# Performance work log

Hardware: AMD Instinct MI355X
Metric: run time of the kernel (lower is better)

## Reference

```python
import jax, jax.numpy as jnp
import numpy as np

EPS = 1e-5
NUM_HEADS = 8

def _bn(x, w, b, m, v):
    # inference-mode BatchNorm2d over channel dim of (B,C,H,W)
    inv = w / jnp.sqrt(v + EPS)
    return x * inv[None, :, None, None] + (b - m * inv)[None, :, None, None]

def _conv1x1(x, W, b):
    # 1x1 conv == per-pixel matmul: W is (out_ch, in_ch)
    return jnp.einsum('bchw,ec->behw', x, W) + b[None, :, None, None]

def _forward(x, bn1_w, bn1_b, bn1_m, bn1_v, Wq, bq, Wk, bk, Wv, bv, gamma, temperature,
             conv_w, conv_b, cbn_w, cbn_b, cbn_m, cbn_v, rs_w, rs_b, rbn_w, rbn_b, rbn_m, rbn_v):
    B, C, Wd, Hd = x.shape
    S = Wd * Hd
    E = Wq.shape[0]
    hd = E // NUM_HEADS
    xa = jax.nn.relu(_bn(x, bn1_w, bn1_b, bn1_m, bn1_v))
    def proj(Wm, bm):
        return _conv1x1(xa, Wm, bm).reshape(B, NUM_HEADS, hd, S).transpose(0, 1, 3, 2)  # (B,h,S,d)
    q = proj(Wq, bq)
    k = proj(Wk, bk)
    v = proj(Wv, bv)
    scores = jnp.einsum('bhsd,bhtd->bhst', q, k) / temperature  # (B,h,S,S)
    scores = scores - jnp.max(scores, axis=-1, keepdims=True)   # redundant amax-subtract as in source
    attn = jax.nn.softmax(scores, axis=-1)
    out = jnp.einsum('bhst,bhtd->bhsd', attn, v)
    out = out.transpose(0, 1, 3, 2).reshape(B, E, Wd, Hd)
    conv_path = jax.nn.relu(_bn(_conv1x1(x, conv_w, conv_b), cbn_w, cbn_b, cbn_m, cbn_v))
    fused = gamma[0] * out + conv_path
    return jax.nn.gelu(_bn(_conv1x1(fused, rs_w, rs_b), rbn_w, rbn_b, rbn_m, rbn_v), approximate=False)

def setup_inputs() -> dict:
    key = jax.random.key(0)
    ks = jax.random.split(key, 18)
    C, E = 256, 512
    n = lambda k, s, sc=0.02: jax.random.normal(k, s, jnp.float32) * sc
    return {
        'x': jax.random.normal(ks[0], (1, C, 64, 64), jnp.float32),
        'bn1_w': 1.0 + n(ks[1], (C,), 0.1), 'bn1_b': n(ks[2], (C,), 0.1),
        'bn1_m': n(ks[3], (C,), 0.05), 'bn1_v': 0.5 + jax.random.uniform(ks[4], (C,), jnp.float32),
        'Wq': n(ks[5], (E, C)), 'bq': jnp.zeros((E,), jnp.float32),
        'Wk': n(ks[6], (E, C)), 'bk': jnp.zeros((E,), jnp.float32),
        'Wv': n(ks[7], (E, C)), 'bv': jnp.zeros((E,), jnp.float32),
        'gamma': jnp.full((1,), 0.5, jnp.float32),
        'temperature': jnp.asarray(0.85, jnp.float32),
        'conv_w': n(ks[8], (E, C)), 'conv_b': jnp.zeros((E,), jnp.float32),
        'cbn_w': 1.0 + n(ks[9], (E,), 0.1), 'cbn_b': n(ks[10], (E,), 0.1),
        'cbn_m': n(ks[11], (E,), 0.05), 'cbn_v': 0.5 + jax.random.uniform(ks[12], (E,), jnp.float32),
        'rs_w': n(ks[13], (C, E)), 'rs_b': jnp.zeros((C,), jnp.float32),
        'rbn_w': 1.0 + n(ks[14], (C,), 0.1), 'rbn_b': n(ks[15], (C,), 0.1),
        'rbn_m': n(ks[16], (C,), 0.05), 'rbn_v': 0.5 + jax.random.uniform(ks[17], (C,), jnp.float32),
    }

def reference(x, bn1_w, bn1_b, bn1_m, bn1_v, Wq, bq, Wk, bk, Wv, bv, gamma, temperature,
              conv_w, conv_b, cbn_w, cbn_b, cbn_m, cbn_v, rs_w, rs_b, rbn_w, rbn_b, rbn_m, rbn_v):
    return _forward(x, bn1_w, bn1_b, bn1_m, bn1_v, Wq, bq, Wk, bk, Wv, bv, gamma, temperature,
                    conv_w, conv_b, cbn_w, cbn_b, cbn_m, cbn_v, rs_w, rs_b, rbn_w, rbn_b, rbn_m, rbn_v)
```

## Files before the change

kernel.cpp:

```cpp
#include <hip/hip_runtime.h>

#define S_DIM 4096
#define C_IN  256
#define E_DIM 512
#define HD    64
#define EPSV  1e-5f

typedef __attribute__((ext_vector_type(8))) short s8v;
typedef __attribute__((ext_vector_type(4))) short s4v;
typedef __attribute__((ext_vector_type(4))) float f4v;
typedef __attribute__((ext_vector_type(16))) float f16v;

__device__ __forceinline__ float bf2f(unsigned short h){
  union{unsigned u; float f;} v; v.u = ((unsigned)h)<<16; return v.f;
}
__device__ __forceinline__ unsigned short f2bf(float f){
  union{float f; unsigned u;} v; v.f = f;
  unsigned r = v.u + 0x7fffu + ((v.u>>16)&1u);
  return (unsigned short)(r>>16);
}
__device__ __forceinline__ unsigned cvtpk_bf16(float lo, float hi_){
  unsigned r;
  asm("v_cvt_pk_bf16_f32 %0, %1, %2" : "=v"(r) : "v"(lo), "v"(hi_));
  return r;
}
__device__ __forceinline__ s8v lds_rd8(const unsigned short* b, int row, int ck){
  return *(const s8v*)&b[(row<<6) + (((ck)^(row&7))<<3)];
}
__device__ __forceinline__ void lds_wr8(unsigned short* b, int row, int ck, s8v v){
  *(s8v*)&b[(row<<6) + (((ck)^(row&7))<<3)] = v;
}
__device__ __forceinline__ s4v lds_rd4q(const unsigned short* b, int row, int q4){
  return *(const s4v*)&b[(row<<6) + (((q4)^(row&15))<<2)];
}
__device__ __forceinline__ void lds_wr4q(unsigned short* b, int row, int q4, s4v v){
  *(s4v*)&b[(row<<6) + (((q4)^(row&15))<<2)] = v;
}

__global__ __launch_bounds__(256) void k_wcvt(const float* __restrict__ w0,
    const float* __restrict__ w1, const float* __restrict__ w2,
    const float* __restrict__ w3, const float* __restrict__ w4,
    unsigned short* __restrict__ dst){
  int i = blockIdx.x*256 + threadIdx.x;
  int z = blockIdx.y;
  const float* s = (z==0)?w0:(z==1)?w1:(z==2)?w2:(z==3)?w3:w4;
  dst[z*(E_DIM*C_IN) + i] = f2bf(s[i]);
}

__global__ __launch_bounds__(256) void k_prep(const float* __restrict__ x,
    const float* __restrict__ bw, const float* __restrict__ bb,
    const float* __restrict__ bm, const float* __restrict__ bvar,
    unsigned short* __restrict__ XaT, unsigned short* __restrict__ XrT){
  __shared__ float tile[32][33];
  int tid = threadIdx.x;
  int tx = tid & 31, ty = tid >> 5;
  int s0 = blockIdx.x*32, c0 = blockIdx.y*32;
  #pragma unroll
  for(int p=0;p<4;p++){
    int c = c0 + ty + p*8;
    tile[ty+p*8][tx] = x[c*S_DIM + s0 + tx];
  }
  __syncthreads();
  int cc = c0 + tx;
  float inv  = bw[cc] * rsqrtf(bvar[cc] + EPSV);
  float beta = bb[cc] - bm[cc]*inv;
  #pragma unroll
  for(int p=0;p<4;p++){
    int s = s0 + ty + p*8;
    float v = tile[tx][ty+p*8];
    float a = v*inv + beta; a = a>0.f?a:0.f;
    XaT[s*C_IN + cc] = f2bf(a);
    XrT[s*C_IN + cc] = f2bf(v);
  }
}

__global__ __launch_bounds__(256) void k_proj(
    const unsigned short* __restrict__ XaT, const unsigned short* __restrict__ XrT,
    const unsigned short* __restrict__ Wb,
    const float* __restrict__ bq, const float* __restrict__ bk,
    const float* __restrict__ bvb, const float* __restrict__ bc,
    const float* __restrict__ cw, const float* __restrict__ cbb,
    const float* __restrict__ cm, const float* __restrict__ cvv,
    unsigned short* __restrict__ QT, unsigned short* __restrict__ KT,
    unsigned short* __restrict__ Vx, unsigned short* __restrict__ CT){
  int z = blockIdx.z;
  const unsigned short* Xin = (z==3) ? XrT : XaT;
  const unsigned short* W   = Wb + z*(E_DIM*C_IN);
  const float* bias = (z==0)?bq:(z==1)?bk:(z==2)?bvb:bc;

  __shared__ unsigned short Als[128*64];
  __shared__ unsigned short Bls[64*64];
  int tid = threadIdx.x;
  int w = tid>>6, l = tid&63, g = l>>4, c16 = l&15;
  int wr = w>>1, wc = w&1;
  int s0 = blockIdx.x*128, e0 = blockIdx.y*64;

  f4v acc[4][2];
  #pragma unroll
  for(int m=0;m<4;m++)
    #pragma unroll
    for(int n=0;n<2;n++) acc[m][n] = (f4v){0.f,0.f,0.f,0.f};

  for(int kk=0;kk<4;kk++){
    __syncthreads();
    #pragma unroll
    for(int p=0;p<4;p++){
      int ck = p*256 + tid, row = ck>>3, ch = ck&7;
      s8v v = *(const s8v*)&Xin[(s0+row)*C_IN + kk*64 + ch*8];
      lds_wr8(Als, row, ch, v);
    }
    #pragma unroll
    for(int p=0;p<2;p++){
      int ck = p*256 + tid, row = ck>>3, ch = ck&7;
      s8v v = *(const s8v*)&W[(e0+row)*C_IN + kk*64 + ch*8];
      lds_wr8(Bls, row, ch, v);
    }
    __syncthreads();
    #pragma unroll
    for(int kb=0;kb<2;kb++){
      s8v bfr[2];
      #pragma unroll
      for(int n=0;n<2;n++) bfr[n] = lds_rd8(Bls, wc*32 + n*16 + c16, g + kb*4);
      #pragma unroll
      for(int m=0;m<4;m++){
        s8v af = lds_rd8(Als, wr*64 + m*16 + c16, g + kb*4);
        #pragma unroll
        for(int n=0;n<2;n++)
          acc[m][n] = __builtin_amdgcn_mfma_f32_16x16x32_bf16(af, bfr[n], acc[m][n], 0,0,0);
      }
    }
  }
  #pragma unroll
  for(int n=0;n<2;n++){
    int e = e0 + wc*32 + n*16 + c16;
    float bsv = bias[e];
    float cinv = 0.f, cbeta = 0.f;
    if(z==3){ cinv = cw[e]*rsqrtf(cvv[e]+EPSV); cbeta = cbb[e] - cm[e]*cinv; }
    #pragma unroll
    for(int m=0;m<4;m++){
      int sb = s0 + wr*64 + m*16 + g*4;
      if(z==2){
        s4v pk;
        #pragma unroll
        for(int i=0;i<4;i++) pk[i] = (short)f2bf(acc[m][n][i] + bsv);
        *(s4v*)&Vx[e*S_DIM + sb] = pk;
      } else {
        unsigned short* dst = (z==0)?QT:(z==1)?KT:CT;
        #pragma unroll
        for(int i=0;i<4;i++){
          float vv = acc[m][n][i] + bsv;
          if(z==3){ vv = vv*cinv + cbeta; vv = vv>0.f?vv:0.f; }
          dst[(sb+i)*E_DIM + e] = f2bf(vv);
        }
      }
    }
  }
}

__global__ __launch_bounds__(256,1) void k_attn(
    const unsigned short* __restrict__ QT, const unsigned short* __restrict__ KT,
    const unsigned short* __restrict__ Vx, const unsigned short* __restrict__ CT,
    const float* __restrict__ gamma, const float* __restrict__ temp,
    unsigned short* __restrict__ fusedT){
  __shared__ unsigned short SM[16384];
  int tid = threadIdx.x;
  int w = tid>>6, l = tid&63, l31 = l&31, hi = l>>5;
  int qh = w&1, kh = w>>1;
  int fb = blockIdx.y*32 + blockIdx.x;
  int h = fb&7;
  int qb = (fb>>3)*128;
  float scl = 1.0f / temp[0];

  const unsigned short* Kb = SM + kh*4096;
  const unsigned short* Vb = SM + 8192 + kh*4096;

  s8v qf[2][4];
  #pragma unroll
  for(int qg=0;qg<2;qg++){
    int q = qb + qh*64 + qg*32 + l31;
    #pragma unroll
    for(int ks=0;ks<4;ks++){
      s8v r = *(const s8v*)&QT[q*E_DIM + h*HD + ks*16 + hi*8];
      #pragma unroll
      for(int j=0;j<8;j++) qf[qg][ks][j] = (short)f2bf(bf2f((unsigned short)r[j])*scl);
    }
  }

  f16v oacc[2][2];
  #pragma unroll
  for(int qg=0;qg<2;qg++)
    #pragma unroll
    for(int dt=0;dt<2;dt++)
      #pragma unroll
      for(int r=0;r<16;r++) oacc[qg][dt][r]=0.f;
  float lrun[2] = {0.f, 0.f};

  int krow = tid>>2, kch2 = (tid&3)*2;
  int vrow = (tid&511)>>3, vch = tid&7;

  s8v kreg[4], vreg[4];
  #pragma unroll
  for(int p=0;p<2;p++){
    #pragma unroll
    for(int kp=0;kp<1;kp++){}
  }
  #pragma unroll
  for(int p=0;p<4;p++){
    int flat = p*256 + tid, kp = flat>>9, cid = flat&511, row = cid>>3, ch = cid&7;
    kreg[p] = *(const s8v*)&KT[((kp*32 + 0)*64 + row)*E_DIM + h*HD + ch*8];
  }
  #pragma unroll
  for(int p=0;p<4;p++){
    int flat = p*256 + tid, kp = flat>>9, cid = flat&511, row = cid>>3, ch = cid&7;
    vreg[p] = *(const s8v*)&Vx[(h*HD + row)*S_DIM + (kp*32 + 0)*64 + ch*8];
  }

  for(int t=0;t<32;t++){
    __syncthreads();
    #pragma unroll
    for(int p=0;p<4;p++){
      int flat = p*256 + tid, kp = flat>>9, cid = flat&511, row = cid>>3, ch = cid&7;
      lds_wr8((unsigned short*)SM + kp*4096, row, ch, kreg[p]);
    }
    #pragma unroll
    for(int p=0;p<4;p++){
      int flat = p*256 + tid, kp = flat>>9, cid = flat&511, row = cid>>3, ch = cid&7;
      union{ s8v v; s4v h2[2]; } u; u.v = vreg[p];
      unsigned short* Vt = (unsigned short*)SM + 8192 + kp*4096;
      lds_wr4q(Vt, row, ch*2,   u.h2[0]);
      lds_wr4q(Vt, row, ch*2+1, u.h2[1]);
    }
    __syncthreads();
    if(t < 31){
      #pragma unroll
      for(int p=0;p<4;p++){
        int flat = p*256 + tid, kp = flat>>9, cid = flat&511, row = cid>>3, ch = cid&7;
        kreg[p] = *(const s8v*)&KT[((kp*32 + t+1)*64 + row)*E_DIM + h*HD + ch*8];
      }
      #pragma unroll
      for(int p=0;p<4;p++){
        int flat = p*256 + tid, kp = flat>>9, cid = flat&511, row = cid>>3, ch = cid&7;
        vreg[p] = *(const s8v*)&Vx[(h*HD + row)*S_DIM + (kp*32 + t+1)*64 + ch*8];
      }
    }

    #pragma unroll
    for(int sub=0;sub<2;sub++){
      int kr = sub*32 + l31;
      s8v kf[4];
      #pragma unroll
      for(int ks=0;ks<4;ks++) kf[ks] = lds_rd8(Kb, kr, ks*2 + hi);

      union{ s8v v; unsigned u[4]; } pa[2][2];
      #pragma unroll
      for(int qg=0;qg<2;qg++){
        f16v d;
        #pragma unroll
        for(int r=0;r<16;r++) d[r]=0.f;
        #pragma unroll
        for(int ks=0;ks<4;ks++)
          d = __builtin_amdgcn_mfma_f32_32x32x16_bf16(kf[ks], qf[qg][ks], d, 0,0,0);
        float e[16], ls = 0.f;
        #pragma unroll
        for(int r=0;r<16;r++){ e[r] = __expf(d[r]); ls += e[r]; }
        lrun[qg] += ls;
        #pragma unroll
        for(int j=0;j<4;j++){
          pa[qg][0].u[j] = cvtpk_bf16(e[2*j],   e[2*j+1]);
          pa[qg][1].u[j] = cvtpk_bf16(e[8+2*j], e[8+2*j+1]);
        }
      }
      #pragma unroll
      for(int dt=0;dt<2;dt++){
        int vr = dt*32 + l31;
        union{ s8v v; s4v h2[2]; } vf;
        vf.h2[0] = lds_rd4q(Vb, vr, sub*8 + hi);
        vf.h2[1] = lds_rd4q(Vb, vr, sub*8 + 2 + hi);
        oacc[0][dt] = __builtin_amdgcn_mfma_f32_32x32x16_bf16(pa[0][0].v, vf.v, oacc[0][dt], 0,0,0);
        oacc[1][dt] = __builtin_amdgcn_mfma_f32_32x32x16_bf16(pa[1][0].v, vf.v, oacc[1][dt], 0,0,0);
        vf.h2[0] = lds_rd4q(Vb, vr, sub*8 + 4 + hi);
        vf.h2[1] = lds_rd4q(Vb, vr, sub*8 + 6 + hi);
        oacc[0][dt] = __builtin_amdgcn_mfma_f32_32x32x16_bf16(pa[0][1].v, vf.v, oacc[0][dt], 0,0,0);
        oacc[1][dt] = __builtin_amdgcn_mfma_f32_32x32x16_bf16(pa[1][1].v, vf.v, oacc[1][dt], 0,0,0);
      }
    }
  }

  #pragma unroll
  for(int qg=0;qg<2;qg++) lrun[qg] += __shfl_xor(lrun[qg], 32);

  float* mb = (float*)SM;
  float* l_buf = mb + 4224;
  float ga = gamma[0];
  #pragma unroll
  for(int qg=0;qg<2;qg++){
    __syncthreads();
    if(kh==1){
      float* dst = mb + (qh*64 + l)*33;
      #pragma unroll
      for(int r=0;r<16;r++){ dst[r] = oacc[qg][0][r]; dst[16+r] = oacc[qg][1][r]; }
      dst[32] = lrun[qg];
    }
    __syncthreads();
    float ltot = 0.f;
    if(kh==0){
      const float* src = mb + (qh*64 + l)*33;
      #pragma unroll
      for(int r=0;r<16;r++){ oacc[qg][0][r] += src[r]; oacc[qg][1][r] += src[16+r]; }
      ltot = lrun[qg] + src[32];
      if(hi==0) l_buf[qh*32 + l31] = ltot;
    }
    __syncthreads();
    if(kh==0){
      #pragma unroll
      for(int dt=0;dt<2;dt++){
        int e = h*HD + dt*32 + l31;
        #pragma unroll
        for(int g4=0;g4<4;g4++){
          float4 lv = *(float4*)&l_buf[qh*32 + g4*8 + hi*4];
          float la[4] = {lv.x, lv.y, lv.z, lv.w};
          #pragma unroll
          for(int j=0;j<4;j++){
            int r = g4*4 + j;
            int qrow = qb + qh*64 + qg*32 + j + g4*8 + hi*4;
            float o = oacc[qg][dt][r]/la[j]*ga + bf2f(CT[qrow*E_DIM + e]);
            fusedT[qrow*E_DIM + e] = f2bf(o);
          }
        }
      }
    }
  }
}

__global__ __launch_bounds__(256) void k_final(
    const unsigned short* __restrict__ Wrs,
    const unsigned short* __restrict__ fusedT,
    const float* __restrict__ rsb,
    const float* __restrict__ rw, const float* __restrict__ rbb,
    const float* __restrict__ rm, const float* __restrict__ rv,
    float* __restrict__ out){
  __shared__ unsigned short Als[64*64];
  __shared__ unsigned short Bls[64*64];
  int tid = threadIdx.x;
  int w = tid>>6, l = tid&63, g = l>>4, c16 = l&15;
  int wr2 = w>>1, wc2 = w&1;
  int sB0 = blockIdx.x*64, c0 = blockIdx.y*64;
  f4v acc[2][2];
  #pragma unroll
  for(int m=0;m<2;m++)
    #pragma unroll
    for(int n=0;n<2;n++) acc[m][n]=(f4v){0.f,0.f,0.f,0.f};
  for(int kk=0;kk<8;kk++){
    __syncthreads();
    #pragma unroll
    for(int p=0;p<2;p++){
      int ck = p*256+tid, row=ck>>3, ch=ck&7;
      s8v v = *(const s8v*)&Wrs[(c0+row)*E_DIM + kk*64 + ch*8];
      lds_wr8(Als, row, ch, v);
    }
    #pragma unroll
    for(int p=0;p<2;p++){
      int ck = p*256+tid, row=ck>>3, ch=ck&7;
      s8v v = *(const s8v*)&fusedT[(sB0+row)*E_DIM + kk*64 + ch*8];
      lds_wr8(Bls, row, ch, v);
    }
    __syncthreads();
    #pragma unroll
    for(int kb=0;kb<2;kb++){
      s8v af[2]; s8v bfr[2];
      #pragma unroll
      for(int m=0;m<2;m++) af[m] = lds_rd8(Als, wr2*32 + m*16 + c16, g + kb*4);
      #pragma unroll
      for(int n=0;n<2;n++) bfr[n] = lds_rd8(Bls, wc2*32 + n*16 + c16, g + kb*4);
      #pragma unroll
      for(int m=0;m<2;m++)
        #pragma unroll
        for(int n=0;n<2;n++)
          acc[m][n] = __builtin_amdgcn_mfma_f32_16x16x32_bf16(af[m], bfr[n], acc[m][n],0,0,0);
    }
  }
  #pragma unroll
  for(int m=0;m<2;m++){
    #pragma unroll
    for(int i=0;i<4;i++){
      int c = c0 + wr2*32 + m*16 + g*4 + i;
      float bias = rsb[c];
      float rinv = rw[c]*rsqrtf(rv[c]+EPSV);
      float rbeta = rbb[c] - rm[c]*rinv;
      #pragma unroll
      for(int n=0;n<2;n++){
        int s = sB0 + wc2*32 + n*16 + c16;
        float vv = acc[m][n][i] + bias;
        vv = vv*rinv + rbeta;
        out[c*S_DIM + s] = 0.5f*vv*(1.0f + erff(vv*0.70710678118f));
      }
    }
  }
}

extern "C" void kernel_launch(void* const* d_in, const int* in_sizes, int n_in,
                              void* d_out, int out_size, void* d_ws, size_t ws_size,
                              hipStream_t stream){
  const float* x     = (const float*)d_in[0];
  const float* bn1w  = (const float*)d_in[1];
  const float* bn1b  = (const float*)d_in[2];
  const float* bn1m  = (const float*)d_in[3];
  const float* bn1v  = (const float*)d_in[4];
  const float* Wq    = (const float*)d_in[5];
  const float* bq    = (const float*)d_in[6];
  const float* Wk    = (const float*)d_in[7];
  const float* bk    = (const float*)d_in[8];
  const float* Wv    = (const float*)d_in[9];
  const float* bv    = (const float*)d_in[10];
  const float* gamma = (const float*)d_in[11];
  const float* temp  = (const float*)d_in[12];
  const float* convw = (const float*)d_in[13];
  const float* convb = (const float*)d_in[14];
  const float* cbnw  = (const float*)d_in[15];
  const float* cbnb  = (const float*)d_in[16];
  const float* cbnm  = (const float*)d_in[17];
  const float* cbnv  = (const float*)d_in[18];
  const float* rsw   = (const float*)d_in[19];
  const float* rsbp  = (const float*)d_in[20];
  const float* rbnw  = (const float*)d_in[21];
  const float* rbnb  = (const float*)d_in[22];
  const float* rbnm  = (const float*)d_in[23];
  const float* rbnv  = (const float*)d_in[24];
  float* out = (float*)d_out;

  unsigned short* ws  = (unsigned short*)d_ws;
  unsigned short* XaT = ws;
  unsigned short* XrT = XaT + S_DIM*C_IN;
  unsigned short* Wb  = XrT + S_DIM*C_IN;
  unsigned short* Wrs = Wb + 4*E_DIM*C_IN;
  unsigned short* QT  = Wrs + C_IN*E_DIM;
  unsigned short* KT  = QT + S_DIM*E_DIM;
  unsigned short* Vx  = KT + S_DIM*E_DIM;
  unsigned short* CT  = Vx + S_DIM*E_DIM;
  unsigned short* fusedT = CT + S_DIM*E_DIM;

  k_wcvt<<<dim3(512,5),256,0,stream>>>(Wq, Wk, Wv, convw, rsw, Wb);
  k_prep<<<dim3(128,8),256,0,stream>>>(x, bn1w, bn1b, bn1m, bn1v, XaT, XrT);
  k_proj<<<dim3(32,8,4),256,0,stream>>>(XaT, XrT, Wb, bq, bk, bv, convb,
                                        cbnw, cbnb, cbnm, cbnv, QT, KT, Vx, CT);
  k_attn<<<dim3(32,8),256,0,stream>>>(QT, KT, Vx, CT, gamma, temp, fusedT);
  k_final<<<dim3(64,4),256,0,stream>>>(Wrs, fusedT, rsbp, rbnw, rbnb, rbnm, rbnv, out);
}
```

Baseline: 94.26 us.

## Restructure attention with direct global-to-LDS double buffering and 4-way key split

The attention kernel now uses 512-thread blocks with four key-split wave groups. K/V tiles are staged straight into double-buffered LDS via global_load_lds, so register staging and the LDS write pass go away. To make the direct copies land in the swizzled layout the readers expect, the projection kernel now writes K and V pre-swizzled in global memory. Softmax switches to exp2 with log2e folded into the scale, and row sums are taken on the matrix units by multiplying with a ones vector. A wider cross-wave reduction is added at the end, and LDS use grows to 128KB per block, which limits occupancy.

```diff
diff --git a/kernel.cpp b/kernel.cpp
--- a/kernel.cpp
+++ b/kernel.cpp
@@ -33,8 +33,10 @@
 __device__ __forceinline__ s4v lds_rd4q(const unsigned short* b, int row, int q4){
   return *(const s4v*)&b[(row<<6) + (((q4)^(row&15))<<2)];
 }
-__device__ __forceinline__ void lds_wr4q(unsigned short* b, int row, int q4, s4v v){
-  *(s4v*)&b[(row<<6) + (((q4)^(row&15))<<2)] = v;
+__device__ __forceinline__ void gl_lds16(const unsigned short* g, unsigned short* l){
+  __builtin_amdgcn_global_load_lds(
+      (const __attribute__((address_space(1))) unsigned int*)g,
+      (__attribute__((address_space(3))) unsigned int*)l, 16, 0, 0);
 }
 
 __global__ __launch_bounds__(256) void k_wcvt(const float* __restrict__ w0,
@@ -143,41 +145,42 @@
         s4v pk;
         #pragma unroll
         for(int i=0;i<4;i++) pk[i] = (short)f2bf(acc[m][n][i] + bsv);
-        *(s4v*)&Vx[e*S_DIM + sb] = pk;
+        int sb2 = (sb & ~63) | ((((sb>>2)&15) ^ (e&15))<<2);
+        *(s4v*)&Vx[e*S_DIM + sb2] = pk;
       } else {
         unsigned short* dst = (z==0)?QT:(z==1)?KT:CT;
         #pragma unroll
         for(int i=0;i<4;i++){
           float vv = acc[m][n][i] + bsv;
           if(z==3){ vv = vv*cinv + cbeta; vv = vv>0.f?vv:0.f; }
-          dst[(sb+i)*E_DIM + e] = f2bf(vv);
+          int key = sb+i;
+          int ee = e;
+          if(z==1) ee = (e & ~56) | ((((e>>3)&7) ^ (key&7))<<3);
+          dst[key*E_DIM + ee] = f2bf(vv);
         }
       }
     }
   }
 }
 
-__global__ __launch_bounds__(256,1) void k_attn(
+__global__ __launch_bounds__(512,2) void k_attn(
     const unsigned short* __restrict__ QT, const unsigned short* __restrict__ KT,
     const unsigned short* __restrict__ Vx, const unsigned short* __restrict__ CT,
     const float* __restrict__ gamma, const float* __restrict__ temp,
     unsigned short* __restrict__ fusedT){
-  __shared__ unsigned short SM[16384];
+  __shared__ unsigned short SM[65536];
   int tid = threadIdx.x;
   int w = tid>>6, l = tid&63, l31 = l&31, hi = l>>5;
-  int qh = w&1, kh = w>>1;
-  int fb = blockIdx.y*32 + blockIdx.x;
-  int h = fb&7;
-  int qb = (fb>>3)*128;
-  float scl = 1.0f / temp[0];
-
-  const unsigned short* Kb = SM + kh*4096;
-  const unsigned short* Vb = SM + 8192 + kh*4096;
+  int qh = w>>2, kh = w&3;
+  int bx = blockIdx.x;
+  int h = bx&7;
+  int q0b = (bx>>3)*128;
+  float scl = 1.4426950408889634f / temp[0];
 
   s8v qf[2][4];
   #pragma unroll
   for(int qg=0;qg<2;qg++){
-    int q = qb + qh*64 + qg*32 + l31;
+    int q = q0b + qh*64 + qg*32 + l31;
     #pragma unroll
     for(int ks=0;ks<4;ks++){
       s8v r = *(const s8v*)&QT[q*E_DIM + h*HD + ks*16 + hi*8];
@@ -185,64 +188,39 @@
       for(int j=0;j<8;j++) qf[qg][ks][j] = (short)f2bf(bf2f((unsigned short)r[j])*scl);
     }
   }
+  s8v ones;
+  #pragma unroll
+  for(int j=0;j<8;j++) ones[j] = (short)0x3F80;
 
   f16v oacc[2][2];
-  #pragma unroll
-  for(int qg=0;qg<2;qg++)
-    #pragma unroll
-    for(int dt=0;dt<2;dt++)
-      #pragma unroll
-      for(int r=0;r<16;r++) oacc[qg][dt][r]=0.f;
-  float lrun[2] = {0.f, 0.f};
-
-  int krow = tid>>2, kch2 = (tid&3)*2;
-  int vrow = (tid&511)>>3, vch = tid&7;
-
-  s8v kreg[4], vreg[4];
-  #pragma unroll
-  for(int p=0;p<2;p++){
-    #pragma unroll
-    for(int kp=0;kp<1;kp++){}
-  }
-  #pragma unroll
-  for(int p=0;p<4;p++){
-    int flat = p*256 + tid, kp = flat>>9, cid = flat&511, row = cid>>3, ch = cid&7;
-    kreg[p] = *(const s8v*)&KT[((kp*32 + 0)*64 + row)*E_DIM + h*HD + ch*8];
-  }
-  #pragma unroll
-  for(int p=0;p<4;p++){
-    int flat = p*256 + tid, kp = flat>>9, cid = flat&511, row = cid>>3, ch = cid&7;
-    vreg[p] = *(const s8v*)&Vx[(h*HD + row)*S_DIM + (kp*32 + 0)*64 + ch*8];
-  }
-
-  for(int t=0;t<32;t++){
-    __syncthreads();
-    #pragma unroll
-    for(int p=0;p<4;p++){
-      int flat = p*256 + tid, kp = flat>>9, cid = flat&511, row = cid>>3, ch = cid&7;
-      lds_wr8((unsigned short*)SM + kp*4096, row, ch, kreg[p]);
-    }
-    #pragma unroll
-    for(int p=0;p<4;p++){
-      int flat = p*256 + tid, kp = flat>>9, cid = flat&511, row = cid>>3, ch = cid&7;
-      union{ s8v v; s4v h2[2]; } u; u.v = vreg[p];
-      unsigned short* Vt = (unsigned short*)SM + 8192 + kp*4096;
-      lds_wr4q(Vt, row, ch*2,   u.h2[0]);
-      lds_wr4q(Vt, row, ch*2+1, u.h2[1]);
-    }
-    __syncthreads();
-    if(t < 31){
-      #pragma unroll
-      for(int p=0;p<4;p++){
-        int flat = p*256 + tid, kp = flat>>9, cid = flat&511, row = cid>>3, ch = cid&7;
-        kreg[p] = *(const s8v*)&KT[((kp*32 + t+1)*64 + row)*E_DIM + h*HD + ch*8];
-      }
-      #pragma unroll
-      for(int p=0;p<4;p++){
-        int flat = p*256 + tid, kp = flat>>9, cid = flat&511, row = cid>>3, ch = cid&7;
-        vreg[p] = *(const s8v*)&Vx[(h*HD + row)*S_DIM + (kp*32 + t+1)*64 + ch*8];
-      }
-    }
+  f16v lacc[2];
+  #pragma unroll
+  for(int qg=0;qg<2;qg++){
+    #pragma unroll
+    for(int r=0;r<16;r++){ oacc[qg][0][r]=0.f; oacc[qg][1][r]=0.f; lacc[qg][r]=0.f; }
+  }
+
+  #define STAGE(BUF, T) { \
+    _Pragma("unroll") \
+    for(int j=0;j<8;j++){ \
+      int flat = (w*8+j)*64 + l; \
+      int tile = flat>>9, gg = flat&511, row = gg>>3, ch = gg&7; \
+      int khp = tile&3; \
+      int sK = khp*1024 + (T)*64; \
+      const unsigned short* src = (tile<4) \
+        ? &KT[(sK+row)*E_DIM + h*HD + ch*8] \
+        : &Vx[(h*HD+row)*S_DIM + sK + ch*8]; \
+      gl_lds16(src, SM + (BUF)*32768 + (w*8+j)*512); \
+    } }
+
+  int buf = 0;
+  STAGE(0, 0);
+  for(int t=0;t<16;t++){
+    asm volatile("s_waitcnt vmcnt(0)" ::: "memory");
+    __syncthreads();
+    if(t<15) STAGE(buf^1, t+1);
+    const unsigned short* Kb = SM + buf*32768 + kh*4096;
+    const unsigned short* Vb = SM + buf*32768 + (4+kh)*4096;
 
     #pragma unroll
     for(int sub=0;sub<2;sub++){
@@ -260,15 +238,16 @@
         #pragma unroll
         for(int ks=0;ks<4;ks++)
           d = __builtin_amdgcn_mfma_f32_32x32x16_bf16(kf[ks], qf[qg][ks], d, 0,0,0);
-        float e[16], ls = 0.f;
-        #pragma unroll
-        for(int r=0;r<16;r++){ e[r] = __expf(d[r]); ls += e[r]; }
-        lrun[qg] += ls;
+        float e_[16];
+        #pragma unroll
+        for(int r=0;r<16;r++) e_[r] = __builtin_amdgcn_exp2f(d[r]);
         #pragma unroll
         for(int j=0;j<4;j++){
-          pa[qg][0].u[j] = cvtpk_bf16(e[2*j],   e[2*j+1]);
-          pa[qg][1].u[j] = cvtpk_bf16(e[8+2*j], e[8+2*j+1]);
+          pa[qg][0].u[j] = cvtpk_bf16(e_[2*j],   e_[2*j+1]);
+          pa[qg][1].u[j] = cvtpk_bf16(e_[8+2*j], e_[8+2*j+1]);
         }
+        lacc[qg] = __builtin_amdgcn_mfma_f32_32x32x16_bf16(pa[qg][0].v, ones, lacc[qg],0,0,0);
+        lacc[qg] = __builtin_amdgcn_mfma_f32_32x32x16_bf16(pa[qg][1].v, ones, lacc[qg],0,0,0);
       }
       #pragma unroll
       for(int dt=0;dt<2;dt++){
@@ -284,52 +263,43 @@
         oacc[1][dt] = __builtin_amdgcn_mfma_f32_32x32x16_bf16(pa[1][1].v, vf.v, oacc[1][dt], 0,0,0);
       }
     }
-  }
-
-  #pragma unroll
-  for(int qg=0;qg<2;qg++) lrun[qg] += __shfl_xor(lrun[qg], 32);
-
-  float* mb = (float*)SM;
-  float* l_buf = mb + 4224;
+    buf ^= 1;
+  }
+
+  float* slab = (float*)SM;
   float ga = gamma[0];
   #pragma unroll
   for(int qg=0;qg<2;qg++){
     __syncthreads();
-    if(kh==1){
-      float* dst = mb + (qh*64 + l)*33;
-      #pragma unroll
-      for(int r=0;r<16;r++){ dst[r] = oacc[qg][0][r]; dst[16+r] = oacc[qg][1][r]; }
-      dst[32] = lrun[qg];
-    }
-    __syncthreads();
-    float ltot = 0.f;
+    if(kh!=0){
+      float* dst = slab + ((qh*3 + (kh-1))*64 + l)*48;
+      #pragma unroll
+      for(int r=0;r<16;r++){
+        dst[r] = oacc[qg][0][r]; dst[16+r] = oacc[qg][1][r]; dst[32+r] = lacc[qg][r];
+      }
+    }
+    __syncthreads();
     if(kh==0){
-      const float* src = mb + (qh*64 + l)*33;
-      #pragma unroll
-      for(int r=0;r<16;r++){ oacc[qg][0][r] += src[r]; oacc[qg][1][r] += src[16+r]; }
-      ltot = lrun[qg] + src[32];
-      if(hi==0) l_buf[qh*32 + l31] = ltot;
-    }
-    __syncthreads();
-    if(kh==0){
-      #pragma unroll
-      for(int dt=0;dt<2;dt++){
-        int e = h*HD + dt*32 + l31;
-        #pragma unroll
-        for(int g4=0;g4<4;g4++){
-          float4 lv = *(float4*)&l_buf[qh*32 + g4*8 + hi*4];
-          float la[4] = {lv.x, lv.y, lv.z, lv.w};
-          #pragma unroll
-          for(int j=0;j<4;j++){
-            int r = g4*4 + j;
-            int qrow = qb + qh*64 + qg*32 + j + g4*8 + hi*4;
-            float o = oacc[qg][dt][r]/la[j]*ga + bf2f(CT[qrow*E_DIM + e]);
-            fusedT[qrow*E_DIM + e] = f2bf(o);
-          }
-        }
-      }
-    }
-  }
+      f16v o0 = oacc[qg][0], o1 = oacc[qg][1], lt = lacc[qg];
+      #pragma unroll
+      for(int s=0;s<3;s++){
+        const float* src = slab + ((qh*3 + s)*64 + l)*48;
+        #pragma unroll
+        for(int r=0;r<16;r++){ o0[r] += src[r]; o1[r] += src[16+r]; lt[r] += src[32+r]; }
+      }
+      #pragma unroll
+      for(int r=0;r<16;r++){
+        int qrow = q0b + qh*64 + qg*32 + (r&3) + 8*(r>>2) + 4*hi;
+        float rl = __builtin_amdgcn_rcpf(lt[r]) * ga;
+        int e0i = h*HD + l31;
+        float oA = o0[r]*rl + bf2f(CT[qrow*E_DIM + e0i]);
+        float oB = o1[r]*rl + bf2f(CT[qrow*E_DIM + e0i + 32]);
+        fusedT[qrow*E_DIM + e0i]      = f2bf(oA);
+        fusedT[qrow*E_DIM + e0i + 32] = f2bf(oB);
+      }
+    }
+  }
+  #undef STAGE
 }
 
 __global__ __launch_bounds__(256) void k_final(
@@ -443,6 +413,6 @@
   k_prep<<<dim3(128,8),256,0,stream>>>(x, bn1w, bn1b, bn1m, bn1v, XaT, XrT);
   k_proj<<<dim3(32,8,4),256,0,stream>>>(XaT, XrT, Wb, bq, bk, bv, convb,
                                         cbnw, cbnb, cbnm, cbnv, QT, KT, Vx, CT);
-  k_attn<<<dim3(32,8),256,0,stream>>>(QT, KT, Vx, CT, gamma, temp, fusedT);
+  k_attn<<<dim3(256),512,0,stream>>>(QT, KT, Vx, CT, gamma, temp, fusedT);
   k_final<<<dim3(64,4),256,0,stream>>>(Wrs, fusedT, rsbp, rbnw, rbnb, rbnm, rbnv, out);
 }
```

After: 87.96 us. 6.7% less time.
